# Kernel tuning notes

Hardware: AMD Instinct MI355X
Metric: run time of the kernel (lower is better)

The kernel has to match this reference:

```python
import jax, jax.numpy as jnp
import numpy as np

NPOINT = 1024
RADIUS = 0.9
NSAMPLE = 32
MLP = [64, 64, 128]
IN_CH = 67
BN_EPS = 1e-5


def setup_inputs() -> dict:
    key = jax.random.key(0)
    ks = jax.random.split(key, 2 + 2 * len(MLP))
    B, N, C = 16, 4096, 64
    inp = {}
    inp["xyz"] = jax.random.uniform(ks[0], (B, N, 3), dtype=jnp.float32)
    inp["points"] = jax.random.normal(ks[1], (B, N, C), dtype=jnp.float32)
    last = IN_CH
    for i, oc in enumerate(MLP):
        inp[f"w{i}"] = jax.random.normal(ks[2 + 2 * i], (oc, last), dtype=jnp.float32) * (1.0 / np.sqrt(last))
        inp[f"b{i}"] = jax.random.normal(ks[3 + 2 * i], (oc,), dtype=jnp.float32) * 0.01
        inp[f"g{i}"] = jnp.ones((oc,), jnp.float32)
        inp[f"beta{i}"] = jnp.zeros((oc,), jnp.float32)
        last = oc
    return inp


def _farthest_point_sample(xyz, npoint):
    # Sequential FPS; initial farthest index fixed to 0 (torch used randint) for determinism.
    B, N, _ = xyz.shape

    def step(carry, _):
        distance, far = carry
        cen = jnp.take_along_axis(xyz, far[:, None, None], axis=1)  # [B,1,3]
        d = jnp.sum((xyz - cen) ** 2, -1)                            # [B,N]
        distance = jnp.minimum(distance, d)
        new_far = jnp.argmax(distance, axis=-1).astype(jnp.int32)
        return (distance, new_far), far

    init = (jnp.full((B, N), 1e10, xyz.dtype), jnp.zeros((B,), jnp.int32))
    _, cents = jax.lax.scan(step, init, None, length=npoint)  # [npoint, B]
    return jnp.transpose(cents)  # [B, npoint]


def _gather(points, idx):
    # points [B,N,C], idx [B,S] or [B,S,K]
    return jax.vmap(lambda p, i: p[i])(points, idx)


def _query_ball_point(radius, nsample, xyz, new_xyz):
    # Faithful to source: Euclidean distance (cdist p=2) compared against radius**2.
    B, N, _ = xyz.shape
    d2 = (jnp.sum(new_xyz ** 2, -1)[:, :, None]
          + jnp.sum(xyz ** 2, -1)[:, None, :]
          - 2.0 * jnp.einsum('bsc,bnc->bsn', new_xyz, xyz))
    dist = jnp.sqrt(jnp.maximum(d2, 0.0))                  # [B,S,N]
    arang = jnp.arange(N, dtype=jnp.int32)[None, None, :]
    gi = jnp.where(dist > radius ** 2, N, arang)           # [B,S,N]
    gi = jnp.sort(gi, axis=-1)[:, :, :nsample]             # [B,S,K]
    first = gi[:, :, :1]
    gi = jnp.where(gi == N, first, gi)
    return gi


def _forward(xyz, points, params):
    idx = _farthest_point_sample(xyz, NPOINT)              # [B,S]
    new_xyz = _gather(xyz, idx)                            # [B,S,3]
    gidx = _query_ball_point(RADIUS, NSAMPLE, xyz, new_xyz)
    grouped_xyz = _gather(xyz, gidx)                       # [B,S,K,3]
    grouped_xyz_norm = grouped_xyz - new_xyz[:, :, None, :]
    grouped_pts = _gather(points, gidx)                    # [B,S,K,C]
    x = jnp.concatenate([grouped_xyz_norm, grouped_pts], axis=-1)  # [B,S,K,3+C]
    x = jnp.transpose(x, (0, 3, 1, 2))                     # [B,Cin,S,K]
    for (w, b, g, be) in params:
        x = jnp.einsum('oc,bcsk->bosk', w, x) + b[None, :, None, None]
        mu = jnp.mean(x, axis=(0, 2, 3), keepdims=True)    # BN in training mode (batch stats, biased var)
        var = jnp.mean((x - mu) ** 2, axis=(0, 2, 3), keepdims=True)
        x = (x - mu) / jnp.sqrt(var + BN_EPS) * g[None, :, None, None] + be[None, :, None, None]
        x = jax.nn.relu(x)
    new_points = jnp.max(x, axis=-1)                       # [B,Cout,S]
    new_points = jnp.transpose(new_points, (0, 2, 1))      # [B,S,Cout]
    return new_xyz, new_points


def reference(xyz, points, w0, b0, g0, beta0, w1, b1, g1, beta1, w2, b2, g2, beta2):
    params = [(w0, b0, g0, beta0), (w1, b1, g1, beta1), (w2, b2, g2, beta2)]
    return _forward(xyz, points, params)
```

## Files before the change

kernel.cpp:

```cpp
#include <hip/hip_runtime.h>
#include <hip/hip_bf16.h>
#include <stdint.h>

#define BB 16
#define NN 4096
#define NPOINT 1024
#define NSAMPLE 32

typedef unsigned int u32;
typedef unsigned long long u64;
typedef unsigned short u16;
typedef float f32x2 __attribute__((ext_vector_type(2)));
using frag_ab = __attribute__((ext_vector_type(8))) short;
using frag_cd = __attribute__((ext_vector_type(4))) float;

__device__ inline u16 f2bf(float x){ u32 u = __float_as_uint(x); u32 r = (u + 0x7fffu + ((u>>16)&1u)) >> 16; return (u16)r; }
__device__ inline float bf2f(u32 hbits){ return __uint_as_float(hbits<<16); }
__device__ inline u64 umax64(u64 a, u64 b){ return a > b ? a : b; }

__device__ inline int wave_max_bits(float v){
    int x = __float_as_int(v);
    int t;
    t = __builtin_amdgcn_update_dpp(0, x, 0x111, 0xf, 0xf, true);
    x = __float_as_int(fmaxf(__int_as_float(x), __int_as_float(t)));
    t = __builtin_amdgcn_update_dpp(0, x, 0x112, 0xf, 0xf, true);
    x = __float_as_int(fmaxf(__int_as_float(x), __int_as_float(t)));
    t = __builtin_amdgcn_update_dpp(0, x, 0x114, 0xf, 0xf, true);
    x = __float_as_int(fmaxf(__int_as_float(x), __int_as_float(t)));
    t = __builtin_amdgcn_update_dpp(0, x, 0x118, 0xf, 0xf, true);
    x = __float_as_int(fmaxf(__int_as_float(x), __int_as_float(t)));
    t = __builtin_amdgcn_update_dpp(0, x, 0x142, 0xf, 0xf, true);
    x = __float_as_int(fmaxf(__int_as_float(x), __int_as_float(t)));
    t = __builtin_amdgcn_update_dpp(0, x, 0x143, 0xf, 0xf, true);
    x = __float_as_int(fmaxf(__int_as_float(x), __int_as_float(t)));
    return __builtin_amdgcn_readlane(x, 63);
}

__global__ __launch_bounds__(256) void fps_kernel(const float* __restrict__ xyz, int* __restrict__ cents)
{
#pragma clang fp contract(off)
    __shared__ float lxyz[NN*3];
    __shared__ __align__(16) u64 s_red[2][4];
    const int tid = threadIdx.x;
    const int b = blockIdx.x;
    const float* gx = xyz + (size_t)b*NN*3;
    for (int i = tid; i < NN*3; i += 256) lxyz[i] = gx[i];
    __syncthreads();
    f32x2 px[8], py[8], pz[8], dist[8];
#pragma unroll
    for (int jj = 0; jj < 8; jj++){
        int p = tid*16 + jj*2;
        px[jj] = (f32x2){ lxyz[p*3+0], lxyz[(p+1)*3+0] };
        py[jj] = (f32x2){ lxyz[p*3+1], lxyz[(p+1)*3+1] };
        pz[jj] = (f32x2){ lxyz[p*3+2], lxyz[(p+1)*3+2] };
        dist[jj] = (f32x2){ 1e10f, 1e10f };
    }
    const int lane = tid & 63;
    const int wid = tid >> 6;
    int far = 0, par = 0;
    for (int s = 0; s < NPOINT; s++){
        if (tid == 0) cents[b*NPOINT + s] = far;
        float cx = lxyz[far*3+0], cy = lxyz[far*3+1], cz = lxyz[far*3+2];
        f32x2 c2x = { cx, cx }, c2y = { cy, cy }, c2z = { cz, cz };
        float bv = -1.0f; int bj = 0;
#pragma unroll
        for (int jj = 0; jj < 8; jj++){
            f32x2 dx = px[jj] - c2x;
            f32x2 dy = py[jj] - c2y;
            f32x2 dz = pz[jj] - c2z;
            f32x2 d  = (dx*dx + dy*dy) + dz*dz;
            f32x2 nd;
            nd.x = fminf(dist[jj].x, d.x);
            nd.y = fminf(dist[jj].y, d.y);
            dist[jj] = nd;
            if (nd.x > bv){ bv = nd.x; bj = jj*2; }
            if (nd.y > bv){ bv = nd.y; bj = jj*2+1; }
        }
        int wmb = wave_max_bits(bv);
        float wmax = __int_as_float(wmb);
        u64 mask = __ballot(bv == wmax);
        int fl = __ffsll((long long)mask) - 1;
        int fj = __builtin_amdgcn_readlane(bj, fl);
        int p = (wid << 10) + (fl << 4) + fj;
        if (lane == 0) s_red[par][wid] = ((u64)(u32)wmb << 32) | (u32)(4095 - p);
        __syncthreads();
        u64 m0 = umax64(s_red[par][0], s_red[par][1]);
        u64 m1 = umax64(s_red[par][2], s_red[par][3]);
        u64 m  = umax64(m0, m1);
        far = 4095 - (int)(m & 0xFFFu);
        par ^= 1;
    }
}

__global__ __launch_bounds__(256) void gather_newxyz_kernel(const float* __restrict__ xyz, const int* __restrict__ cents,
                                                            float* __restrict__ out, float* __restrict__ nxyz)
{
    int i = blockIdx.x*256 + threadIdx.x;
    int b = i / 3072;
    int r = i - b*3072;
    int s = r / 3;
    int c = r - s*3;
    int idx = cents[b*NPOINT + s];
    float v = xyz[((size_t)b*NN + idx)*3 + c];
    out[i] = v;
    nxyz[i] = v;
}

__global__ __launch_bounds__(256) void pack_points_kernel(const float* __restrict__ points, u32* __restrict__ pbf)
{
    int i = blockIdx.x*256 + threadIdx.x;
    float f0 = points[2*i], f1 = points[2*i+1];
    pbf[i] = (u32)f2bf(f0) | ((u32)f2bf(f1) << 16);
}

__global__ __launch_bounds__(256) void ballquery_kernel(const float* __restrict__ xyz, const float* __restrict__ nxyz,
                                                        const int* __restrict__ cents, int* __restrict__ gidx)
{
    const int lane = threadIdx.x & 63;
    const int w = (blockIdx.x << 2) + (threadIdx.x >> 6);
    const int b = w >> 10;
    const float RAD2 = (float)(0.9*0.9);
    const float* c3 = nxyz + (size_t)w*3;
    float cx = c3[0], cy = c3[1], cz = c3[2];
    float sc = __fadd_rn(__fadd_rn(__fmul_rn(cx,cx), __fmul_rn(cy,cy)), __fmul_rn(cz,cz));
    const float* gx = xyz + (size_t)b*NN*3;
    int* gout = gidx + (size_t)w*NSAMPLE;
    int found = 0; int first = -1;
    for (int base = 0; base < NN; base += 64){
        int i = base + lane;
        float pxv = gx[i*3+0], pyv = gx[i*3+1], pzv = gx[i*3+2];
        float sp = __fadd_rn(__fadd_rn(__fmul_rn(pxv,pxv), __fmul_rn(pyv,pyv)), __fmul_rn(pzv,pzv));
        float dot = __fadd_rn(__fadd_rn(__fmul_rn(cx,pxv), __fmul_rn(cy,pyv)), __fmul_rn(cz,pzv));
        float d2 = __fsub_rn(__fadd_rn(sc, sp), __fmul_rn(2.0f, dot));
        float dd = __fsqrt_rn(fmaxf(d2, 0.0f));
        bool in = !(dd > RAD2);
        u64 m = __ballot(in);
        int cnt = __popcll(m);
        if (in){
            int slot = found + __popcll(m & ((1ull<<lane) - 1ull));
            if (slot < NSAMPLE) gout[slot] = i;
        }
        if (found == 0 && cnt > 0) first = base + (__ffsll(m) - 1);
        found += cnt;
        if (found >= NSAMPLE) break;
    }
    if (found < NSAMPLE){
        if (found == 0) first = cents[w];
        for (int slot = found + lane; slot < NSAMPLE; slot += 64) gout[slot] = first;
    }
}

__global__ __launch_bounds__(256) void conv1_kernel(const float* __restrict__ xyz, const u32* __restrict__ pbf,
                                                    const float* __restrict__ nxyz, const int* __restrict__ gidx,
                                                    const float* __restrict__ w, const float* __restrict__ bias,
                                                    u32* __restrict__ xout, float* __restrict__ stats)
{
    __shared__ float sxyz[512][3];
    const int tid = threadIdx.x;
    const int lane = tid & 63;
    const int wid = tid >> 6;
    const int quad = lane >> 4;
    const int col = lane & 15;
    const int blockbase = blockIdx.x*512;
    for (int r = tid; r < 512; r += 256){
        int m = blockbase + r;
        int b = m >> 15, s = (m >> 5) & 1023, g = gidx[m];
        const float* p3 = xyz + ((size_t)(b<<12) + g)*3;
        const float* c3 = nxyz + ((size_t)b*NPOINT + s)*3;
        sxyz[r][0] = p3[0]-c3[0]; sxyz[r][1] = p3[1]-c3[1]; sxyz[r][2] = p3[2]-c3[2];
    }
    frag_ab Bf[4][2];
#pragma unroll
    for (int nt = 0; nt < 4; nt++)
#pragma unroll
        for (int kh = 0; kh < 2; kh++){
            const float* wr = w + (nt*16 + col)*67 + 3 + kh*32 + quad*8;
#pragma unroll
            for (int j = 0; j < 8; j++) Bf[nt][kh][j] = (short)f2bf(wr[j]);
        }
    float wx[4], wy[4], wz[4], biasl[4];
#pragma unroll
    for (int nt = 0; nt < 4; nt++){
        const float* wb = w + (nt*16 + col)*67;
        wx[nt] = wb[0]; wy[nt] = wb[1]; wz[nt] = wb[2];
        biasl[nt] = bias[nt*16 + col];
    }
    __syncthreads();
    float ssum[4] = {0,0,0,0}, ssq[4] = {0,0,0,0};
    u16* xo = (u16*)xout;
    const int tile0 = blockIdx.x*32 + wid*8;
#pragma unroll 2
    for (int t = 0; t < 8; t++){
        const int tile = tile0 + t;
        const size_t m0 = (size_t)tile * 16;
        const int b = (int)(m0 >> 15);
        const int g = gidx[m0 + col];
        const u32* arow = pbf + ((size_t)(b<<12) + g)*32;
        uint4 u0 = *(const uint4*)(arow + quad*4);
        uint4 u1 = *(const uint4*)(arow + 16 + quad*4);
        frag_ab Af0, Af1;
        __builtin_memcpy(&Af0, &u0, 16);
        __builtin_memcpy(&Af1, &u1, 16);
        frag_cd acc[4];
#pragma unroll
        for (int nt = 0; nt < 4; nt++){
            acc[nt] = (frag_cd){0.f, 0.f, 0.f, 0.f};
            acc[nt] = __builtin_amdgcn_mfma_f32_16x16x32_bf16(Af0, Bf[nt][0], acc[nt], 0, 0, 0);
            acc[nt] = __builtin_amdgcn_mfma_f32_16x16x32_bf16(Af1, Bf[nt][1], acc[nt], 0, 0, 0);
        }
        const int rbase = (int)(m0 - blockbase) + quad*4;
#pragma unroll
        for (int r = 0; r < 4; r++){
            float xnx = sxyz[rbase+r][0], xny = sxyz[rbase+r][1], xnz = sxyz[rbase+r][2];
#pragma unroll
            for (int nt = 0; nt < 4; nt++){
                float v = acc[nt][r] + biasl[nt];
                v = fmaf(wx[nt], xnx, v);
                v = fmaf(wy[nt], xny, v);
                v = fmaf(wz[nt], xnz, v);
                xo[(m0 + quad*4 + r)*64 + nt*16 + col] = f2bf(v);
                ssum[nt] += v;
                ssq[nt] = fmaf(v, v, ssq[nt]);
            }
        }
    }
#pragma unroll
    for (int nt = 0; nt < 4; nt++){
        ssum[nt] += __shfl_xor(ssum[nt], 16); ssq[nt] += __shfl_xor(ssq[nt], 16);
        ssum[nt] += __shfl_xor(ssum[nt], 32); ssq[nt] += __shfl_xor(ssq[nt], 32);
    }
    if (quad == 0){
        float* st = stats + (blockIdx.x & 7)*256;
#pragma unroll
        for (int nt = 0; nt < 4; nt++){
            atomicAdd(&st[nt*16 + col], ssum[nt]);
            atomicAdd(&st[128 + nt*16 + col], ssq[nt]);
        }
    }
}

__device__ inline void block_finalize(const float* __restrict__ stats, const float* __restrict__ g,
                                      const float* __restrict__ beta, float* saff, int C, int tid)
{
    if (tid < C){
        float sm = 0.f, sq = 0.f;
#pragma unroll
        for (int r = 0; r < 8; r++){ sm += stats[r*256+tid]; sq += stats[r*256+128+tid]; }
        const float invM = 1.0f / 524288.0f;
        float mu  = sm * invM;
        float var = fmaxf(sq * invM - mu*mu, 0.0f);
        float inv = 1.0f / sqrtf(var + 1e-5f);
        float a = g[tid] * inv;
        saff[tid] = a;
        saff[128+tid] = beta[tid] - mu*a;
    }
}

__device__ inline void unpack_affine_relu(uint4 u, const float* ak, const float* bk, short* dst){
    const u32* uu = (const u32*)&u;
#pragma unroll
    for (int q = 0; q < 4; q++){
        u32 v = uu[q];
        float x0 = bf2f(v & 0xffffu);
        float x1 = bf2f(v >> 16);
        float f0 = fmaxf(fmaf(ak[2*q],   x0, bk[2*q]),   0.f);
        float f1 = fmaxf(fmaf(ak[2*q+1], x1, bk[2*q+1]), 0.f);
        dst[2*q]   = (short)f2bf(f0);
        dst[2*q+1] = (short)f2bf(f1);
    }
}

__global__ __launch_bounds__(256) void conv2_kernel(const u32* __restrict__ xin, const float* __restrict__ stats_in,
                                                    const float* __restrict__ gw, const float* __restrict__ beta,
                                                    const float* __restrict__ w, const float* __restrict__ bias,
                                                    u32* __restrict__ xout, float* __restrict__ stats)
{
    __shared__ float saff[256];
    const int tid = threadIdx.x;
    block_finalize(stats_in, gw, beta, saff, 64, tid);
    const int lane = tid & 63;
    const int wid = tid >> 6;
    const int quad = lane >> 4;
    const int col = lane & 15;
    frag_ab Bf[4][2];
#pragma unroll
    for (int nt = 0; nt < 4; nt++)
#pragma unroll
        for (int kh = 0; kh < 2; kh++){
            const float* wr = w + (nt*16 + col)*64 + kh*32 + quad*8;
#pragma unroll
            for (int j = 0; j < 8; j++) Bf[nt][kh][j] = (short)f2bf(wr[j]);
        }
    float biasl[4];
#pragma unroll
    for (int nt = 0; nt < 4; nt++) biasl[nt] = bias[nt*16 + col];
    __syncthreads();
    float ak[2][8], bk[2][8];
#pragma unroll
    for (int kh = 0; kh < 2; kh++)
#pragma unroll
        for (int j = 0; j < 8; j++){
            int k = kh*32 + quad*8 + j;
            ak[kh][j] = saff[k]; bk[kh][j] = saff[128+k];
        }
    float ssum[4] = {0,0,0,0}, ssq[4] = {0,0,0,0};
    u16* xo = (u16*)xout;
    const int tile0 = blockIdx.x*64 + wid*16;
    for (int t = 0; t < 16; t++){
        const size_t m0 = (size_t)(tile0 + t) * 16;
        const u32* arow = xin + (m0 + col)*32;
        uint4 u0 = *(const uint4*)(arow + quad*4);
        uint4 u1 = *(const uint4*)(arow + 16 + quad*4);
        frag_ab Af0, Af1;
        unpack_affine_relu(u0, ak[0], bk[0], (short*)&Af0);
        unpack_affine_relu(u1, ak[1], bk[1], (short*)&Af1);
        frag_cd acc[4];
#pragma unroll
        for (int nt = 0; nt < 4; nt++){
            acc[nt] = (frag_cd){biasl[nt], biasl[nt], biasl[nt], biasl[nt]};
            acc[nt] = __builtin_amdgcn_mfma_f32_16x16x32_bf16(Af0, Bf[nt][0], acc[nt], 0, 0, 0);
            acc[nt] = __builtin_amdgcn_mfma_f32_16x16x32_bf16(Af1, Bf[nt][1], acc[nt], 0, 0, 0);
        }
#pragma unroll
        for (int nt = 0; nt < 4; nt++){
#pragma unroll
            for (int r = 0; r < 4; r++){
                float v = acc[nt][r];
                xo[(m0 + quad*4 + r)*64 + nt*16 + col] = f2bf(v);
                ssum[nt] += v;
                ssq[nt] = fmaf(v, v, ssq[nt]);
            }
        }
    }
#pragma unroll
    for (int nt = 0; nt < 4; nt++){
        ssum[nt] += __shfl_xor(ssum[nt], 16); ssq[nt] += __shfl_xor(ssq[nt], 16);
        ssum[nt] += __shfl_xor(ssum[nt], 32); ssq[nt] += __shfl_xor(ssq[nt], 32);
    }
    if (quad == 0){
        float* st = stats + (blockIdx.x & 7)*256;
#pragma unroll
        for (int nt = 0; nt < 4; nt++){
            atomicAdd(&st[nt*16 + col], ssum[nt]);
            atomicAdd(&st[128 + nt*16 + col], ssq[nt]);
        }
    }
}

__global__ __launch_bounds__(256) void conv3_kernel(const u32* __restrict__ xin, const float* __restrict__ stats_in,
                                                    const float* __restrict__ gw, const float* __restrict__ beta,
                                                    const float* __restrict__ w, const float* __restrict__ bias,
                                                    float* __restrict__ gmax, float* __restrict__ gmin,
                                                    float* __restrict__ stats)
{
    __shared__ float saff[256];
    const int tid = threadIdx.x;
    block_finalize(stats_in, gw, beta, saff, 64, tid);
    const int lane = tid & 63;
    const int wid = tid >> 6;
    const int quad = lane >> 4;
    const int col = lane & 15;
    frag_ab Bf[8][2];
#pragma unroll
    for (int nt = 0; nt < 8; nt++)
#pragma unroll
        for (int kh = 0; kh < 2; kh++){
            const float* wr = w + (nt*16 + col)*64 + kh*32 + quad*8;
#pragma unroll
            for (int j = 0; j < 8; j++) Bf[nt][kh][j] = (short)f2bf(wr[j]);
        }
    float biasl[8];
#pragma unroll
    for (int nt = 0; nt < 8; nt++) biasl[nt] = bias[nt*16 + col];
    __syncthreads();
    float ak[2][8], bk[2][8];
#pragma unroll
    for (int kh = 0; kh < 2; kh++)
#pragma unroll
        for (int j = 0; j < 8; j++){
            int k = kh*32 + quad*8 + j;
            ak[kh][j] = saff[k]; bk[kh][j] = saff[128+k];
        }
    float ssum[8], ssq[8], mx[8], mn[8];
#pragma unroll
    for (int nt = 0; nt < 8; nt++){ ssum[nt] = 0.f; ssq[nt] = 0.f; }
    const int tile0 = blockIdx.x*32 + wid*8;
#pragma unroll 2
    for (int t = 0; t < 8; t++){
        const size_t m0 = (size_t)(tile0 + t) * 16;
        const u32* arow = xin + (m0 + col)*32;
        uint4 u0 = *(const uint4*)(arow + quad*4);
        uint4 u1 = *(const uint4*)(arow + 16 + quad*4);
        frag_ab Af0, Af1;
        unpack_affine_relu(u0, ak[0], bk[0], (short*)&Af0);
        unpack_affine_relu(u1, ak[1], bk[1], (short*)&Af1);
        frag_cd acc[8];
#pragma unroll
        for (int nt = 0; nt < 8; nt++){
            acc[nt] = (frag_cd){biasl[nt], biasl[nt], biasl[nt], biasl[nt]};
            acc[nt] = __builtin_amdgcn_mfma_f32_16x16x32_bf16(Af0, Bf[nt][0], acc[nt], 0, 0, 0);
            acc[nt] = __builtin_amdgcn_mfma_f32_16x16x32_bf16(Af1, Bf[nt][1], acc[nt], 0, 0, 0);
        }
#pragma unroll
        for (int nt = 0; nt < 8; nt++){
            float a0 = fmaxf(fmaxf(acc[nt][0], acc[nt][1]), fmaxf(acc[nt][2], acc[nt][3]));
            float n0 = fminf(fminf(acc[nt][0], acc[nt][1]), fminf(acc[nt][2], acc[nt][3]));
            if ((t & 1) == 0){ mx[nt] = a0; mn[nt] = n0; }
            else { mx[nt] = fmaxf(mx[nt], a0); mn[nt] = fminf(mn[nt], n0); }
#pragma unroll
            for (int r = 0; r < 4; r++){
                float v = acc[nt][r];
                ssum[nt] += v;
                ssq[nt] = fmaf(v, v, ssq[nt]);
            }
        }
        if (t & 1){
#pragma unroll
            for (int nt = 0; nt < 8; nt++){
                mx[nt] = fmaxf(mx[nt], __shfl_xor(mx[nt], 16));
                mn[nt] = fminf(mn[nt], __shfl_xor(mn[nt], 16));
                mx[nt] = fmaxf(mx[nt], __shfl_xor(mx[nt], 32));
                mn[nt] = fminf(mn[nt], __shfl_xor(mn[nt], 32));
            }
            if (quad == 0){
                const int g = (tile0 + t - 1) >> 1;
#pragma unroll
                for (int nt = 0; nt < 8; nt++){
                    gmax[(size_t)g*128 + nt*16 + col] = mx[nt];
                    gmin[(size_t)g*128 + nt*16 + col] = mn[nt];
                }
            }
        }
    }
#pragma unroll
    for (int nt = 0; nt < 8; nt++){
        ssum[nt] += __shfl_xor(ssum[nt], 16); ssq[nt] += __shfl_xor(ssq[nt], 16);
        ssum[nt] += __shfl_xor(ssum[nt], 32); ssq[nt] += __shfl_xor(ssq[nt], 32);
    }
    if (quad == 0){
        float* st = stats + (blockIdx.x & 7)*256;
#pragma unroll
        for (int nt = 0; nt < 8; nt++){
            atomicAdd(&st[nt*16 + col], ssum[nt]);
            atomicAdd(&st[128 + nt*16 + col], ssq[nt]);
        }
    }
}

__global__ __launch_bounds__(256) void pool_kernel(const float* __restrict__ gmax, const float* __restrict__ gmin,
                                                   const float* __restrict__ stats_in, const float* __restrict__ gw,
                                                   const float* __restrict__ beta, float* __restrict__ out)
{
    __shared__ float saff[256];
    const int tid = threadIdx.x;
    block_finalize(stats_in, gw, beta, saff, 128, tid);
    __syncthreads();
    const int base = blockIdx.x*2048 + tid;
#pragma unroll
    for (int k = 0; k < 8; k++){
        int idx = base + k*256;
        int o = idx & 127;
        float a = saff[o], bsh = saff[128+o];
        float v = (a >= 0.f) ? fmaf(a, gmax[idx], bsh) : fmaf(a, gmin[idx], bsh);
        out[(size_t)BB*NPOINT*3 + idx] = fmaxf(v, 0.f);
    }
}

extern "C" void kernel_launch(void* const* d_in, const int* in_sizes, int n_in,
                              void* d_out, int out_size, void* d_ws, size_t ws_size,
                              hipStream_t stream)
{
    const float* xyz    = (const float*)d_in[0];
    const float* points = (const float*)d_in[1];
    const float* w0  = (const float*)d_in[2];
    const float* b0  = (const float*)d_in[3];
    const float* g0  = (const float*)d_in[4];
    const float* be0 = (const float*)d_in[5];
    const float* w1  = (const float*)d_in[6];
    const float* b1  = (const float*)d_in[7];
    const float* g1  = (const float*)d_in[8];
    const float* be1 = (const float*)d_in[9];
    const float* w2  = (const float*)d_in[10];
    const float* b2  = (const float*)d_in[11];
    const float* g2  = (const float*)d_in[12];
    const float* be2 = (const float*)d_in[13];
    float* out = (float*)d_out;
    char* ws = (char*)d_ws;

    int*   cents = (int*)(ws + 0);
    float* nxyz  = (float*)(ws + 65536);
    int*   gidx  = (int*)(ws + 262144);
    float* stats = (float*)(ws + 2359296);
    u32*   x1buf = (u32*)(ws + 2386944);
    u32*   x2buf = (u32*)(ws + 69495808);
    float* gmax  = (float*)(ws + 136604672);
    float* gmin  = (float*)(ws + 144993280);
    u32*   pbf   = (u32*)(ws + 136604672);

    hipMemsetAsync(stats, 0, 6144*sizeof(float), stream);
    fps_kernel<<<16, 256, 0, stream>>>(xyz, cents);
    gather_newxyz_kernel<<<192, 256, 0, stream>>>(xyz, cents, out, nxyz);
    pack_points_kernel<<<8192, 256, 0, stream>>>(points, pbf);
    ballquery_kernel<<<4096, 256, 0, stream>>>(xyz, nxyz, cents, gidx);
    conv1_kernel<<<1024, 256, 0, stream>>>(xyz, pbf, nxyz, gidx, w0, b0, x1buf, stats);
    conv2_kernel<<<512, 256, 0, stream>>>(x1buf, stats, g0, be0, w1, b1, x2buf, stats + 2048);
    conv3_kernel<<<1024, 256, 0, stream>>>(x2buf, stats + 2048, g1, be1, w2, b2, gmax, gmin, stats + 4096);
    pool_kernel<<<1024, 256, 0, stream>>>(gmax, gmin, stats + 4096, g2, be2, out);
}
```

Baseline: 760.0 us.

## Fuse FPS, point packing, ball query and conv1 into a persistent producer-consumer kernel

```diff
diff --git a/kernel.cpp b/kernel.cpp
--- a/kernel.cpp
+++ b/kernel.cpp
@@ -36,205 +36,185 @@
     return __builtin_amdgcn_readlane(x, 63);
 }
 
-__global__ __launch_bounds__(256) void fps_kernel(const float* __restrict__ xyz, int* __restrict__ cents)
+__global__ __launch_bounds__(256) void mega_kernel(const float* __restrict__ xyz, const float* __restrict__ points,
+    const float* __restrict__ w0, const float* __restrict__ bias0,
+    int* __restrict__ cents, u32* __restrict__ pbf, int* __restrict__ gidx,
+    float* __restrict__ out, float* __restrict__ stats,
+    int* __restrict__ progress, int* __restrict__ packdone, u32* __restrict__ x1buf)
 {
 #pragma clang fp contract(off)
     __shared__ float lxyz[NN*3];
     __shared__ __align__(16) u64 s_red[2][4];
     const int tid = threadIdx.x;
-    const int b = blockIdx.x;
-    const float* gx = xyz + (size_t)b*NN*3;
-    for (int i = tid; i < NN*3; i += 256) lxyz[i] = gx[i];
-    __syncthreads();
-    f32x2 px[8], py[8], pz[8], dist[8];
-#pragma unroll
-    for (int jj = 0; jj < 8; jj++){
-        int p = tid*16 + jj*2;
-        px[jj] = (f32x2){ lxyz[p*3+0], lxyz[(p+1)*3+0] };
-        py[jj] = (f32x2){ lxyz[p*3+1], lxyz[(p+1)*3+1] };
-        pz[jj] = (f32x2){ lxyz[p*3+2], lxyz[(p+1)*3+2] };
-        dist[jj] = (f32x2){ 1e10f, 1e10f };
-    }
     const int lane = tid & 63;
     const int wid = tid >> 6;
-    int far = 0, par = 0;
-    for (int s = 0; s < NPOINT; s++){
-        if (tid == 0) cents[b*NPOINT + s] = far;
-        float cx = lxyz[far*3+0], cy = lxyz[far*3+1], cz = lxyz[far*3+2];
-        f32x2 c2x = { cx, cx }, c2y = { cy, cy }, c2z = { cz, cz };
-        float bv = -1.0f; int bj = 0;
+
+    if (blockIdx.x < 16){
+        const int b = blockIdx.x;
+        const float* gx = xyz + (size_t)b*NN*3;
+        for (int i = tid; i < NN*3; i += 256) lxyz[i] = gx[i];
+        __syncthreads();
+        f32x2 px[8], py[8], pz[8], dist[8];
 #pragma unroll
         for (int jj = 0; jj < 8; jj++){
-            f32x2 dx = px[jj] - c2x;
-            f32x2 dy = py[jj] - c2y;
-            f32x2 dz = pz[jj] - c2z;
-            f32x2 d  = (dx*dx + dy*dy) + dz*dz;
-            f32x2 nd;
-            nd.x = fminf(dist[jj].x, d.x);
-            nd.y = fminf(dist[jj].y, d.y);
-            dist[jj] = nd;
-            if (nd.x > bv){ bv = nd.x; bj = jj*2; }
-            if (nd.y > bv){ bv = nd.y; bj = jj*2+1; }
-        }
-        int wmb = wave_max_bits(bv);
-        float wmax = __int_as_float(wmb);
-        u64 mask = __ballot(bv == wmax);
-        int fl = __ffsll((long long)mask) - 1;
-        int fj = __builtin_amdgcn_readlane(bj, fl);
-        int p = (wid << 10) + (fl << 4) + fj;
-        if (lane == 0) s_red[par][wid] = ((u64)(u32)wmb << 32) | (u32)(4095 - p);
+            int p = tid*16 + jj*2;
+            px[jj] = (f32x2){ lxyz[p*3+0], lxyz[(p+1)*3+0] };
+            py[jj] = (f32x2){ lxyz[p*3+1], lxyz[(p+1)*3+1] };
+            pz[jj] = (f32x2){ lxyz[p*3+2], lxyz[(p+1)*3+2] };
+            dist[jj] = (f32x2){ 1e10f, 1e10f };
+        }
+        int far = 0, par = 0;
+        for (int s = 0; s < NPOINT; s++){
+            if (tid == 0){
+                cents[b*NPOINT + s] = far;
+                if ((s & 15) == 15)
+                    __hip_atomic_store(&progress[b], s + 1, __ATOMIC_RELEASE, __HIP_MEMORY_SCOPE_AGENT);
+            }
+            float cx = lxyz[far*3+0], cy = lxyz[far*3+1], cz = lxyz[far*3+2];
+            f32x2 c2x = { cx, cx }, c2y = { cy, cy }, c2z = { cz, cz };
+            float bv = -1.0f; int bj = 0;
+#pragma unroll
+            for (int jj = 0; jj < 8; jj++){
+                f32x2 dx = px[jj] - c2x;
+                f32x2 dy = py[jj] - c2y;
+                f32x2 dz = pz[jj] - c2z;
+                f32x2 d  = (dx*dx + dy*dy) + dz*dz;
+                f32x2 nd;
+                nd.x = fminf(dist[jj].x, d.x);
+                nd.y = fminf(dist[jj].y, d.y);
+                dist[jj] = nd;
+                if (nd.x > bv){ bv = nd.x; bj = jj*2; }
+                if (nd.y > bv){ bv = nd.y; bj = jj*2+1; }
+            }
+            int wmb = wave_max_bits(bv);
+            float wmax = __int_as_float(wmb);
+            u64 mask = __ballot(bv == wmax);
+            int fl = __ffsll((long long)mask) - 1;
+            int fj = __builtin_amdgcn_readlane(bj, fl);
+            int p = (wid << 10) + (fl << 4) + fj;
+            if (lane == 0) s_red[par][wid] = ((u64)(u32)wmb << 32) | (u32)(4095 - p);
+            __syncthreads();
+            u64 m0 = umax64(s_red[par][0], s_red[par][1]);
+            u64 m1 = umax64(s_red[par][2], s_red[par][3]);
+            u64 m  = umax64(m0, m1);
+            far = 4095 - (int)(m & 0xFFFu);
+            par ^= 1;
+        }
+    } else {
+        const int wi = blockIdx.x - 16;
+        for (int i = wi*256 + tid; i < BB*NN*32; i += 240*256){
+            float f0 = points[2*i], f1 = points[2*i+1];
+            pbf[i] = (u32)f2bf(f0) | ((u32)f2bf(f1) << 16);
+        }
         __syncthreads();
-        u64 m0 = umax64(s_red[par][0], s_red[par][1]);
-        u64 m1 = umax64(s_red[par][2], s_red[par][3]);
-        u64 m  = umax64(m0, m1);
-        far = 4095 - (int)(m & 0xFFFu);
-        par ^= 1;
-    }
-}
-
-__global__ __launch_bounds__(256) void gather_newxyz_kernel(const float* __restrict__ xyz, const int* __restrict__ cents,
-                                                            float* __restrict__ out, float* __restrict__ nxyz)
-{
-    int i = blockIdx.x*256 + threadIdx.x;
-    int b = i / 3072;
-    int r = i - b*3072;
-    int s = r / 3;
-    int c = r - s*3;
-    int idx = cents[b*NPOINT + s];
-    float v = xyz[((size_t)b*NN + idx)*3 + c];
-    out[i] = v;
-    nxyz[i] = v;
-}
-
-__global__ __launch_bounds__(256) void pack_points_kernel(const float* __restrict__ points, u32* __restrict__ pbf)
-{
-    int i = blockIdx.x*256 + threadIdx.x;
-    float f0 = points[2*i], f1 = points[2*i+1];
-    pbf[i] = (u32)f2bf(f0) | ((u32)f2bf(f1) << 16);
-}
-
-__global__ __launch_bounds__(256) void ballquery_kernel(const float* __restrict__ xyz, const float* __restrict__ nxyz,
-                                                        const int* __restrict__ cents, int* __restrict__ gidx)
-{
-    const int lane = threadIdx.x & 63;
-    const int w = (blockIdx.x << 2) + (threadIdx.x >> 6);
-    const int b = w >> 10;
-    const float RAD2 = (float)(0.9*0.9);
-    const float* c3 = nxyz + (size_t)w*3;
-    float cx = c3[0], cy = c3[1], cz = c3[2];
-    float sc = __fadd_rn(__fadd_rn(__fmul_rn(cx,cx), __fmul_rn(cy,cy)), __fmul_rn(cz,cz));
-    const float* gx = xyz + (size_t)b*NN*3;
-    int* gout = gidx + (size_t)w*NSAMPLE;
-    int found = 0; int first = -1;
-    for (int base = 0; base < NN; base += 64){
-        int i = base + lane;
-        float pxv = gx[i*3+0], pyv = gx[i*3+1], pzv = gx[i*3+2];
-        float sp = __fadd_rn(__fadd_rn(__fmul_rn(pxv,pxv), __fmul_rn(pyv,pyv)), __fmul_rn(pzv,pzv));
-        float dot = __fadd_rn(__fadd_rn(__fmul_rn(cx,pxv), __fmul_rn(cy,pyv)), __fmul_rn(cz,pzv));
-        float d2 = __fsub_rn(__fadd_rn(sc, sp), __fmul_rn(2.0f, dot));
-        float dd = __fsqrt_rn(fmaxf(d2, 0.0f));
-        bool in = !(dd > RAD2);
-        u64 m = __ballot(in);
-        int cnt = __popcll(m);
-        if (in){
-            int slot = found + __popcll(m & ((1ull<<lane) - 1ull));
-            if (slot < NSAMPLE) gout[slot] = i;
-        }
-        if (found == 0 && cnt > 0) first = base + (__ffsll(m) - 1);
-        found += cnt;
-        if (found >= NSAMPLE) break;
-    }
-    if (found < NSAMPLE){
-        if (found == 0) first = cents[w];
-        for (int slot = found + lane; slot < NSAMPLE; slot += 64) gout[slot] = first;
-    }
-}
-
-__global__ __launch_bounds__(256) void conv1_kernel(const float* __restrict__ xyz, const u32* __restrict__ pbf,
-                                                    const float* __restrict__ nxyz, const int* __restrict__ gidx,
-                                                    const float* __restrict__ w, const float* __restrict__ bias,
-                                                    u32* __restrict__ xout, float* __restrict__ stats)
-{
-    __shared__ float sxyz[512][3];
-    const int tid = threadIdx.x;
-    const int lane = tid & 63;
-    const int wid = tid >> 6;
-    const int quad = lane >> 4;
-    const int col = lane & 15;
-    const int blockbase = blockIdx.x*512;
-    for (int r = tid; r < 512; r += 256){
-        int m = blockbase + r;
-        int b = m >> 15, s = (m >> 5) & 1023, g = gidx[m];
-        const float* p3 = xyz + ((size_t)(b<<12) + g)*3;
-        const float* c3 = nxyz + ((size_t)b*NPOINT + s)*3;
-        sxyz[r][0] = p3[0]-c3[0]; sxyz[r][1] = p3[1]-c3[1]; sxyz[r][2] = p3[2]-c3[2];
-    }
-    frag_ab Bf[4][2];
-#pragma unroll
-    for (int nt = 0; nt < 4; nt++)
-#pragma unroll
-        for (int kh = 0; kh < 2; kh++){
-            const float* wr = w + (nt*16 + col)*67 + 3 + kh*32 + quad*8;
-#pragma unroll
-            for (int j = 0; j < 8; j++) Bf[nt][kh][j] = (short)f2bf(wr[j]);
-        }
-    float wx[4], wy[4], wz[4], biasl[4];
-#pragma unroll
-    for (int nt = 0; nt < 4; nt++){
-        const float* wb = w + (nt*16 + col)*67;
-        wx[nt] = wb[0]; wy[nt] = wb[1]; wz[nt] = wb[2];
-        biasl[nt] = bias[nt*16 + col];
-    }
-    __syncthreads();
-    float ssum[4] = {0,0,0,0}, ssq[4] = {0,0,0,0};
-    u16* xo = (u16*)xout;
-    const int tile0 = blockIdx.x*32 + wid*8;
-#pragma unroll 2
-    for (int t = 0; t < 8; t++){
-        const int tile = tile0 + t;
-        const size_t m0 = (size_t)tile * 16;
-        const int b = (int)(m0 >> 15);
-        const int g = gidx[m0 + col];
-        const u32* arow = pbf + ((size_t)(b<<12) + g)*32;
-        uint4 u0 = *(const uint4*)(arow + quad*4);
-        uint4 u1 = *(const uint4*)(arow + 16 + quad*4);
-        frag_ab Af0, Af1;
-        __builtin_memcpy(&Af0, &u0, 16);
-        __builtin_memcpy(&Af1, &u1, 16);
-        frag_cd acc[4];
+        if (tid == 0){ __threadfence(); atomicAdd(packdone, 1); }
+        const int quad = lane >> 4;
+        const int col = lane & 15;
+        frag_ab Bf[4][2];
+#pragma unroll
+        for (int nt = 0; nt < 4; nt++)
+#pragma unroll
+            for (int kh = 0; kh < 2; kh++){
+                const float* wr = w0 + (nt*16 + col)*67 + 3 + kh*32 + quad*8;
+#pragma unroll
+                for (int j = 0; j < 8; j++) Bf[nt][kh][j] = (short)f2bf(wr[j]);
+            }
+        float wx[4], wy[4], wz[4], biasl[4];
 #pragma unroll
         for (int nt = 0; nt < 4; nt++){
-            acc[nt] = (frag_cd){0.f, 0.f, 0.f, 0.f};
-            acc[nt] = __builtin_amdgcn_mfma_f32_16x16x32_bf16(Af0, Bf[nt][0], acc[nt], 0, 0, 0);
-            acc[nt] = __builtin_amdgcn_mfma_f32_16x16x32_bf16(Af1, Bf[nt][1], acc[nt], 0, 0, 0);
-        }
-        const int rbase = (int)(m0 - blockbase) + quad*4;
-#pragma unroll
-        for (int r = 0; r < 4; r++){
-            float xnx = sxyz[rbase+r][0], xny = sxyz[rbase+r][1], xnz = sxyz[rbase+r][2];
+            const float* wb = w0 + (nt*16 + col)*67;
+            wx[nt] = wb[0]; wy[nt] = wb[1]; wz[nt] = wb[2];
+            biasl[nt] = bias0[nt*16 + col];
+        }
+        while (__hip_atomic_load(packdone, __ATOMIC_ACQUIRE, __HIP_MEMORY_SCOPE_AGENT) < 240)
+            __builtin_amdgcn_s_sleep(10);
+        float ssum[4] = {0,0,0,0}, ssq[4] = {0,0,0,0};
+        u16* xo = (u16*)x1buf;
+        const float RAD2 = (float)(0.9*0.9);
+        const int wwave = wi*4 + wid;
+        for (int g = wwave; g < BB*NPOINT; g += 960){
+            const int b = g >> 10, s = g & 1023;
+            while (__hip_atomic_load(&progress[b], __ATOMIC_ACQUIRE, __HIP_MEMORY_SCOPE_AGENT) <= s)
+                __builtin_amdgcn_s_sleep(10);
+            const int ci = cents[b*NPOINT + s];
+            const float* cp = xyz + ((size_t)b*NN + ci)*3;
+            float cx = cp[0], cy = cp[1], cz = cp[2];
+            if (lane < 3) out[g*3 + lane] = cp[lane];
+            float sc = __fadd_rn(__fadd_rn(__fmul_rn(cx,cx), __fmul_rn(cy,cy)), __fmul_rn(cz,cz));
+            const float* gx = xyz + (size_t)b*NN*3;
+            int* gout = gidx + (size_t)g*NSAMPLE;
+            int found = 0; int first = -1;
+            for (int base = 0; base < NN; base += 64){
+                int i = base + lane;
+                float pxv = gx[i*3+0], pyv = gx[i*3+1], pzv = gx[i*3+2];
+                float sp = __fadd_rn(__fadd_rn(__fmul_rn(pxv,pxv), __fmul_rn(pyv,pyv)), __fmul_rn(pzv,pzv));
+                float dot = __fadd_rn(__fadd_rn(__fmul_rn(cx,pxv), __fmul_rn(cy,pyv)), __fmul_rn(cz,pzv));
+                float d2 = __fsub_rn(__fadd_rn(sc, sp), __fmul_rn(2.0f, dot));
+                float dd = __fsqrt_rn(fmaxf(d2, 0.0f));
+                bool in = !(dd > RAD2);
+                u64 m = __ballot(in);
+                int cnt = __popcll(m);
+                if (in){
+                    int slot = found + __popcll(m & ((1ull<<lane) - 1ull));
+                    if (slot < NSAMPLE) gout[slot] = i;
+                }
+                if (found == 0 && cnt > 0) first = base + (__ffsll(m) - 1);
+                found += cnt;
+                if (found >= NSAMPLE) break;
+            }
+            if (found < NSAMPLE){
+                if (found == 0) first = ci;
+                for (int slot = found + lane; slot < NSAMPLE; slot += 64) gout[slot] = first;
+            }
+            __threadfence();
+#pragma unroll
+            for (int t = 0; t < 2; t++){
+                const int m0 = g*32 + t*16;
+                const int gg = gidx[m0 + col];
+                const u32* arow = pbf + ((size_t)(b<<12) + gg)*32;
+                uint4 u0 = *(const uint4*)(arow + quad*4);
+                uint4 u1 = *(const uint4*)(arow + 16 + quad*4);
+                frag_ab Af0, Af1;
+                __builtin_memcpy(&Af0, &u0, 16);
+                __builtin_memcpy(&Af1, &u1, 16);
+                frag_cd acc[4];
+#pragma unroll
+                for (int nt = 0; nt < 4; nt++){
+                    acc[nt] = (frag_cd){0.f, 0.f, 0.f, 0.f};
+                    acc[nt] = __builtin_amdgcn_mfma_f32_16x16x32_bf16(Af0, Bf[nt][0], acc[nt], 0, 0, 0);
+                    acc[nt] = __builtin_amdgcn_mfma_f32_16x16x32_bf16(Af1, Bf[nt][1], acc[nt], 0, 0, 0);
+                }
+#pragma unroll
+                for (int r = 0; r < 4; r++){
+                    const int rowm = m0 + quad*4 + r;
+                    const int pt = gidx[rowm];
+                    const float* p3 = xyz + ((size_t)(b<<12) + pt)*3;
+                    float xnx = p3[0]-cx, xny = p3[1]-cy, xnz = p3[2]-cz;
+#pragma unroll
+                    for (int nt = 0; nt < 4; nt++){
+                        float v = acc[nt][r] + biasl[nt];
+                        v = fmaf(wx[nt], xnx, v);
+                        v = fmaf(wy[nt], xny, v);
+                        v = fmaf(wz[nt], xnz, v);
+                        xo[(size_t)rowm*64 + nt*16 + col] = f2bf(v);
+                        ssum[nt] += v;
+                        ssq[nt] = fmaf(v, v, ssq[nt]);
+                    }
+                }
+            }
+        }
+#pragma unroll
+        for (int nt = 0; nt < 4; nt++){
+            ssum[nt] += __shfl_xor(ssum[nt], 16); ssq[nt] += __shfl_xor(ssq[nt], 16);
+            ssum[nt] += __shfl_xor(ssum[nt], 32); ssq[nt] += __shfl_xor(ssq[nt], 32);
+        }
+        if (quad == 0){
+            float* st = stats + (wi & 7)*256;
 #pragma unroll
             for (int nt = 0; nt < 4; nt++){
-                float v = acc[nt][r] + biasl[nt];
-                v = fmaf(wx[nt], xnx, v);
-                v = fmaf(wy[nt], xny, v);
-                v = fmaf(wz[nt], xnz, v);
-                xo[(m0 + quad*4 + r)*64 + nt*16 + col] = f2bf(v);
-                ssum[nt] += v;
-                ssq[nt] = fmaf(v, v, ssq[nt]);
-            }
-        }
-    }
-#pragma unroll
-    for (int nt = 0; nt < 4; nt++){
-        ssum[nt] += __shfl_xor(ssum[nt], 16); ssq[nt] += __shfl_xor(ssq[nt], 16);
-        ssum[nt] += __shfl_xor(ssum[nt], 32); ssq[nt] += __shfl_xor(ssq[nt], 32);
-    }
-    if (quad == 0){
-        float* st = stats + (blockIdx.x & 7)*256;
-#pragma unroll
-        for (int nt = 0; nt < 4; nt++){
-            atomicAdd(&st[nt*16 + col], ssum[nt]);
-            atomicAdd(&st[128 + nt*16 + col], ssq[nt]);
+                atomicAdd(&st[nt*16 + col], ssum[nt]);
+                atomicAdd(&st[128 + nt*16 + col], ssq[nt]);
+            }
         }
     }
 }
@@ -487,22 +467,20 @@
     float* out = (float*)d_out;
     char* ws = (char*)d_ws;
 
-    int*   cents = (int*)(ws + 0);
-    float* nxyz  = (float*)(ws + 65536);
-    int*   gidx  = (int*)(ws + 262144);
-    float* stats = (float*)(ws + 2359296);
-    u32*   x1buf = (u32*)(ws + 2386944);
-    u32*   x2buf = (u32*)(ws + 69495808);
-    float* gmax  = (float*)(ws + 136604672);
-    float* gmin  = (float*)(ws + 144993280);
-    u32*   pbf   = (u32*)(ws + 136604672);
-
-    hipMemsetAsync(stats, 0, 6144*sizeof(float), stream);
-    fps_kernel<<<16, 256, 0, stream>>>(xyz, cents);
-    gather_newxyz_kernel<<<192, 256, 0, stream>>>(xyz, cents, out, nxyz);
-    pack_points_kernel<<<8192, 256, 0, stream>>>(points, pbf);
-    ballquery_kernel<<<4096, 256, 0, stream>>>(xyz, nxyz, cents, gidx);
-    conv1_kernel<<<1024, 256, 0, stream>>>(xyz, pbf, nxyz, gidx, w0, b0, x1buf, stats);
+    int*   cents    = (int*)(ws + 0);
+    int*   gidx     = (int*)(ws + 262144);
+    float* stats    = (float*)(ws + 2359296);
+    int*   progress = (int*)(ws + 2383872);
+    int*   packdone = (int*)(ws + 2383936);
+    u32*   x1buf    = (u32*)(ws + 2386944);
+    u32*   x2buf    = (u32*)(ws + 69495808);
+    float* gmax     = (float*)(ws + 136604672);
+    float* gmin     = (float*)(ws + 144993280);
+    u32*   pbf      = (u32*)(ws + 136604672);
+
+    hipMemsetAsync(ws + 2359296, 0, 24576 + 128, stream);
+    mega_kernel<<<256, 256, 0, stream>>>(xyz, points, w0, b0, cents, pbf, gidx, out,
+                                         stats, progress, packdone, x1buf);
     conv2_kernel<<<512, 256, 0, stream>>>(x1buf, stats, g0, be0, w1, b1, x2buf, stats + 2048);
     conv3_kernel<<<1024, 256, 0, stream>>>(x2buf, stats + 2048, g1, be1, w2, b2, gmax, gmin, stats + 4096);
     pool_kernel<<<1024, 256, 0, stream>>>(gmax, gmin, stats + 4096, g2, be2, out);
```

New measurement: 1.324 ms. +74.2%, slower.
